# Performance work log

Hardware: AMD Instinct MI355X
Metric: run time of the kernel (lower is better)

Reference implementation:

```python
import jax, jax.numpy as jnp
import numpy as np
import math

B, T, C = 2, 2048, 1024
H = 16
D = C // H


def setup_inputs() -> dict:
    key = jax.random.key(0)
    ks = jax.random.split(key, 5)
    s = 1.0 / math.sqrt(C)
    return {
        "x": jax.random.normal(ks[0], (B, T, C), dtype=jnp.float32),
        "W_qkv": jax.random.normal(ks[1], (C, 3 * C), dtype=jnp.float32) * s,
        "b_qkv": jnp.zeros((3 * C,), dtype=jnp.float32),
        "W_proj": jax.random.normal(ks[2], (C, C), dtype=jnp.float32) * s,
        "b_proj": jnp.zeros((C,), dtype=jnp.float32),
    }


def reference(x, W_qkv, b_qkv, W_proj, b_proj):
    qkv = x @ W_qkv + b_qkv  # [B,T,3C]
    q, k, v = jnp.split(qkv, 3, axis=-1)
    # [B,T,C] -> [B,H,T,D]
    q = q.reshape(B, T, H, D).transpose(0, 2, 1, 3)
    k = k.reshape(B, T, H, D).transpose(0, 2, 1, 3)
    v = v.reshape(B, T, H, D).transpose(0, 2, 1, 3)
    sm_scale = 1.0 / math.sqrt(D)
    att = jnp.einsum("bhqd,bhkd->bhqk", q, k) * sm_scale
    causal = jnp.tril(jnp.ones((T, T), dtype=bool))  # True = keep
    att = jnp.where(causal, att, -jnp.inf)
    att = jax.nn.softmax(att, axis=-1)
    y = jnp.einsum("bhqk,bhkd->bhqd", att, v)  # [B,H,T,D]
    y = y.transpose(0, 2, 1, 3).reshape(B, T, C)
    return y @ W_proj + b_proj
```

## Files before the change

### kernel.cpp

```cpp
#include <hip/hip_runtime.h>
#include <hip/hip_bf16.h>
#include <math.h>

#define BB 2
#define TT 2048
#define CCH 1024
#define HH 16
#define DD 64
#define BT (BB*TT)
#define N3 (3*CCH)

typedef __attribute__((ext_vector_type(8))) short short8;
typedef __attribute__((ext_vector_type(4))) float f32x4;
typedef __attribute__((ext_vector_type(16))) float f32x16;

__device__ __forceinline__ unsigned short f2bf(float f) {
  unsigned int u = __float_as_uint(f);
  unsigned int r = (u + 0x7FFFu + ((u >> 16) & 1u)) >> 16;
  return (unsigned short)r;
}
__device__ __forceinline__ int cvtpk(float lo, float hi) {
  int r;
  asm("v_cvt_pk_bf16_f32 %0, %1, %2" : "=v"(r) : "v"(lo), "v"(hi));
  return r;
}
__device__ __forceinline__ void plswap(int &a, int &b) {
  asm("v_permlane32_swap_b32 %0, %1" : "+v"(a), "+v"(b));
}
__device__ __forceinline__ float fexp2(float x) {
  float r;
  asm("v_exp_f32 %0, %1" : "=v"(r) : "v"(x));
  return r;
}
__device__ __forceinline__ void gload_lds16(const unsigned short* g, unsigned short* l) {
  __builtin_amdgcn_global_load_lds((const __attribute__((address_space(1))) void*)g,
                                   (__attribute__((address_space(3))) void*)l, 16, 0, 0);
}
__device__ __forceinline__ float fmax3(float a, float b, float c) {
  return fmaxf(fmaxf(a, b), c);
}


__global__ __launch_bounds__(256) void k_convert(const float* __restrict__ in,
                                                 unsigned short* __restrict__ out, int n8) {
  int i = blockIdx.x * 256 + threadIdx.x;
  if (i < n8) {
    const float4 a = *(const float4*)(in + (size_t)i * 8);
    const float4 b = *(const float4*)(in + (size_t)i * 8 + 4);
    short8 v;
    v[0] = f2bf(a.x); v[1] = f2bf(a.y); v[2] = f2bf(a.z); v[3] = f2bf(a.w);
    v[4] = f2bf(b.x); v[5] = f2bf(b.y); v[6] = f2bf(b.z); v[7] = f2bf(b.w);
    *(short8*)(out + (size_t)i * 8) = v;
  }
}

__global__ __launch_bounds__(256) void k_transpose_cvt(const float* __restrict__ in,
                                                       unsigned short* __restrict__ out,
                                                       int R, int Cn) {
  __shared__ float tile[32][33];
  int tc = blockIdx.x * 32;
  int tr = blockIdx.y * 32;
  int lx = threadIdx.x & 31;
  int ly = threadIdx.x >> 5;
#pragma unroll
  for (int i = 0; i < 32; i += 8)
    tile[ly + i][lx] = in[(size_t)(tr + ly + i) * Cn + tc + lx];
  __syncthreads();
#pragma unroll
  for (int i = 0; i < 32; i += 8)
    out[(size_t)(tc + ly + i) * R + tr + lx] = f2bf(tile[lx][ly + i]);
}

__global__ __launch_bounds__(256) void k_qkv_gemm(const unsigned short* __restrict__ Xb,
                                                  const unsigned short* __restrict__ Wt,
                                                  const float* __restrict__ bias,
                                                  unsigned short* __restrict__ Qf,
                                                  unsigned short* __restrict__ Kf,
                                                  unsigned short* __restrict__ Vf) {
  __shared__ __align__(16) unsigned short As[128 * 32];
  __shared__ __align__(16) unsigned short Bs[128 * 32];
  int tid = threadIdx.x;
  int mb = blockIdx.x * 128;
  int nb = blockIdx.y * 128;
  int wid = tid >> 6, lane = tid & 63;
  int wr = (wid >> 1) * 64, wc = (wid & 1) * 64;
  int l15 = lane & 15, l4 = lane >> 4;
  int l16 = lane >> 2, lc = (lane & 3) * 8;
  f32x4 acc[4][4];
#pragma unroll
  for (int a = 0; a < 4; ++a)
#pragma unroll
    for (int b = 0; b < 4; ++b)
#pragma unroll
      for (int j = 0; j < 4; ++j) acc[a][b][j] = 0.0f;

  for (int kb = 0; kb < CCH; kb += 32) {
#pragma unroll
    for (int i = 0; i < 2; ++i) {
      int arow = wid * 32 + i * 16;
      gload_lds16(Xb + (size_t)(mb + arow + l16) * CCH + kb + lc, &As[arow * 32]);
      gload_lds16(Wt + (size_t)(nb + arow + l16) * CCH + kb + lc, &Bs[arow * 32]);
    }
    __syncthreads();
    short8 af[4], bfr[4];
#pragma unroll
    for (int mt = 0; mt < 4; ++mt) af[mt] = *(const short8*)(&As[(wr + mt * 16 + l15) * 32 + l4 * 8]);
#pragma unroll
    for (int nt = 0; nt < 4; ++nt) bfr[nt] = *(const short8*)(&Bs[(wc + nt * 16 + l15) * 32 + l4 * 8]);
#pragma unroll
    for (int mt = 0; mt < 4; ++mt)
#pragma unroll
      for (int nt = 0; nt < 4; ++nt)
        acc[mt][nt] = __builtin_amdgcn_mfma_f32_16x16x32_bf16(af[mt], bfr[nt], acc[mt][nt], 0, 0, 0);
    __syncthreads();
  }

#pragma unroll
  for (int mt = 0; mt < 4; ++mt) {
#pragma unroll
    for (int nt = 0; nt < 4; ++nt) {
      int gcol = nb + wc + nt * 16 + l15;
      int which = gcol >> 10;
      int cc = gcol & 1023;
      int hh = cc >> 6, d = cc & 63;
      float bv = bias[gcol];
#pragma unroll
      for (int j = 0; j < 4; ++j) {
        int grow = mb + wr + mt * 16 + l4 * 4 + j;
        int b = grow >> 11, t = grow & 2047;
        float v = acc[mt][nt][j] + bv;
        size_t bh = (size_t)(b * HH + hh) * TT * DD;
        if (which == 2) {
          size_t a = (size_t)((((t >> 6) * 2 + (d >> 5)) * 4 + ((t >> 4) & 3)) * 512
                             + (((t >> 3) & 1) * 32 + (d & 31)) * 8 + (t & 7));
          Vf[bh + a] = f2bf(v);
        } else {
          size_t a = (size_t)(((t >> 5) * 4 + (d >> 4)) * 512
                             + ((d >> 3) & 1) * 256 + (t & 31) * 8 + (d & 7));
          if (which == 0) Qf[bh + a] = f2bf(v * 0.18033688f);
          else            Kf[bh + a] = f2bf(v);
        }
      }
    }
  }
}

__global__ __launch_bounds__(128) void k_attn(const unsigned short* __restrict__ Qf,
                                              const unsigned short* __restrict__ Kf,
                                              const unsigned short* __restrict__ Vf,
                                              unsigned short* __restrict__ Y) {
  __shared__ float ex[64 * 33];
  __shared__ float exml[128];
  int tid = threadIdx.x;
  int jx = blockIdx.x;
  int j = 63 - (jx >> 5);
  int bh = jx & 31;
  int wid = tid >> 6, lane = tid & 63;
  int l31 = lane & 31, h = lane >> 5;
  int q0 = j * 32;
  int qrow = q0 + l31;
  int tmax = j >> 1;

  const unsigned short* Qp = Qf + (size_t)bh * TT * DD;
  const unsigned short* Kp = Kf + (size_t)bh * TT * DD;
  const unsigned short* Vp = Vf + (size_t)bh * TT * DD;

  short8 qf[4];
#pragma unroll
  for (int m = 0; m < 4; ++m)
    qf[m] = *(const short8*)(Qp + (size_t)(j * 4 + m) * 512 + lane * 8);

  f32x16 zv;
#pragma unroll
  for (int r = 0; r < 16; ++r) zv[r] = 0.0f;
  f32x16 po[2];
  po[0] = zv; po[1] = zv;
  float mrun = -1e30f, lrun = 0.0f;

  for (int t = wid; t <= tmax; t += 2) {
    int kvb = t * 64;

    short8 kf[2][4];
#pragma unroll
    for (int t32 = 0; t32 < 2; ++t32)
#pragma unroll
      for (int m = 0; m < 4; ++m)
        kf[t32][m] = *(const short8*)(Kp + (size_t)((t * 2 + t32) * 4 + m) * 512 + lane * 8);

    f32x16 st[2];
    __builtin_amdgcn_s_setprio(1);
#pragma unroll
    for (int t32 = 0; t32 < 2; ++t32) {
      st[t32] = __builtin_amdgcn_mfma_f32_32x32x16_bf16(kf[t32][0], qf[0], zv, 0, 0, 0);
#pragma unroll
      for (int m = 1; m < 4; ++m)
        st[t32] = __builtin_amdgcn_mfma_f32_32x32x16_bf16(kf[t32][m], qf[m], st[t32], 0, 0, 0);
    }
    __builtin_amdgcn_s_setprio(0);

    short8 vf[2][4];
#pragma unroll
    for (int dt = 0; dt < 2; ++dt)
#pragma unroll
      for (int g = 0; g < 4; ++g)
        vf[dt][g] = *(const short8*)(Vp + (size_t)((t * 2 + dt) * 4 + g) * 512 + lane * 8);

    if (kvb + 63 > q0) {
#pragma unroll
      for (int t32 = 0; t32 < 2; ++t32)
#pragma unroll
        for (int r = 0; r < 16; ++r) {
          int kvg = kvb + t32 * 32 + (r & 3) + 8 * (r >> 2) + 4 * h;
          if (kvg > qrow) st[t32][r] = -1e30f;
        }
    }

    float A = st[0][0], B = st[0][1], C = st[0][2], Dv = st[0][3];
#pragma unroll
    for (int r = 4; r < 16; r += 4) {
      A = fmax3(A, st[0][r], st[0][r + 1]);
      B = fmax3(B, st[0][r + 2], st[0][r + 3]);
      C = fmax3(C, st[1][r - 4], st[1][r - 3]);
      Dv = fmax3(Dv, st[1][r - 2], st[1][r - 1]);
    }
    C = fmax3(C, st[1][12], st[1][13]);
    Dv = fmax3(Dv, st[1][14], st[1][15]);
    float mx = fmaxf(fmax3(A, B, C), Dv);
    mx = fmaxf(mx, __shfl_xor(mx, 32));

    if (__any(mx - mrun > 8.0f)) {
      float mnew = fmaxf(mrun, mx);
      float alpha = fexp2(mrun - mnew);
      lrun *= alpha;
#pragma unroll
      for (int dt = 0; dt < 2; ++dt)
#pragma unroll
        for (int r = 0; r < 16; ++r) po[dt][r] *= alpha;
      mrun = mnew;
    }

    float sum = 0.0f;
#pragma unroll
    for (int t32 = 0; t32 < 2; ++t32)
#pragma unroll
      for (int r = 0; r < 16; ++r) {
        float p = fexp2(st[t32][r] - mrun);
        st[t32][r] = p;
        sum += p;
      }
    sum += __shfl_xor(sum, 32);
    lrun += sum;

    short8 pf[4];
#pragma unroll
    for (int g = 0; g < 4; ++g) {
      int t32 = g >> 1, r0 = (g & 1) * 8;
      int a = cvtpk(st[t32][r0 + 0], st[t32][r0 + 1]);
      int b = cvtpk(st[t32][r0 + 4], st[t32][r0 + 5]);
      plswap(a, b);
      int c = cvtpk(st[t32][r0 + 2], st[t32][r0 + 3]);
      int d = cvtpk(st[t32][r0 + 6], st[t32][r0 + 7]);
      plswap(c, d);
      union { int w[4]; short8 s; } un;
      un.w[0] = a; un.w[1] = c; un.w[2] = b; un.w[3] = d;
      pf[g] = un.s;
    }

    __builtin_amdgcn_s_setprio(1);
#pragma unroll
    for (int dt = 0; dt < 2; ++dt)
#pragma unroll
      for (int g = 0; g < 4; ++g)
        po[dt] = __builtin_amdgcn_mfma_f32_32x32x16_bf16(vf[dt][g], pf[g], po[dt], 0, 0, 0);
    __builtin_amdgcn_s_setprio(0);
  }

  __syncthreads();
  if (wid == 1) {
#pragma unroll
    for (int dt = 0; dt < 2; ++dt)
#pragma unroll
      for (int r = 0; r < 16; ++r) ex[lane * 33 + dt * 16 + r] = po[dt][r];
    exml[lane] = mrun;
    exml[64 + lane] = lrun;
  }
  __syncthreads();
  if (wid == 0) {
    float m1 = exml[lane], l1 = exml[64 + lane];
    float M = fmaxf(mrun, m1);
    float a0 = fexp2(mrun - M), a1 = fexp2(m1 - M);
    float inv = 1.0f / (lrun * a0 + l1 * a1);
    a0 *= inv; a1 *= inv;
    int b = bh >> 4, hh = bh & 15;
    unsigned short* yp = Y + ((size_t)(b * TT + qrow)) * CCH + hh * DD;
#pragma unroll
    for (int dt = 0; dt < 2; ++dt)
#pragma unroll
      for (int r = 0; r < 16; r += 2) {
        int d = dt * 32 + (r & 3) + 8 * (r >> 2) + 4 * h;
        float v0 = po[dt][r]     * a0 + ex[lane * 33 + dt * 16 + r]     * a1;
        float v1 = po[dt][r + 1] * a0 + ex[lane * 33 + dt * 16 + r + 1] * a1;
        *(int*)(yp + d) = cvtpk(v0, v1);
      }
  }
}

__global__ __launch_bounds__(256) void k_proj_gemm(const unsigned short* __restrict__ Yb,
                                                   const unsigned short* __restrict__ Wt,
                                                   const float* __restrict__ bias,
                                                   float* __restrict__ Out) {
  __shared__ __align__(16) unsigned short As[128 * 32];
  __shared__ __align__(16) unsigned short Bs[128 * 32];
  int tid = threadIdx.x;
  int mb = blockIdx.x * 128;
  int nb = blockIdx.y * 128;
  int wid = tid >> 6, lane = tid & 63;
  int wr = (wid >> 1) * 64, wc = (wid & 1) * 64;
  int l15 = lane & 15, l4 = lane >> 4;
  int l16 = lane >> 2, lc = (lane & 3) * 8;
  f32x4 acc[4][4];
#pragma unroll
  for (int a = 0; a < 4; ++a)
#pragma unroll
    for (int b = 0; b < 4; ++b)
#pragma unroll
      for (int j = 0; j < 4; ++j) acc[a][b][j] = 0.0f;

  for (int kb = 0; kb < CCH; kb += 32) {
#pragma unroll
    for (int i = 0; i < 2; ++i) {
      int arow = wid * 32 + i * 16;
      gload_lds16(Yb + (size_t)(mb + arow + l16) * CCH + kb + lc, &As[arow * 32]);
      gload_lds16(Wt + (size_t)(nb + arow + l16) * CCH + kb + lc, &Bs[arow * 32]);
    }
    __syncthreads();
    short8 af[4], bfr[4];
#pragma unroll
    for (int mt = 0; mt < 4; ++mt) af[mt] = *(const short8*)(&As[(wr + mt * 16 + l15) * 32 + l4 * 8]);
#pragma unroll
    for (int nt = 0; nt < 4; ++nt) bfr[nt] = *(const short8*)(&Bs[(wc + nt * 16 + l15) * 32 + l4 * 8]);
#pragma unroll
    for (int mt = 0; mt < 4; ++mt)
#pragma unroll
      for (int nt = 0; nt < 4; ++nt)
        acc[mt][nt] = __builtin_amdgcn_mfma_f32_16x16x32_bf16(af[mt], bfr[nt], acc[mt][nt], 0, 0, 0);
    __syncthreads();
  }

#pragma unroll
  for (int mt = 0; mt < 4; ++mt) {
#pragma unroll
    for (int nt = 0; nt < 4; ++nt) {
      int gcol = nb + wc + nt * 16 + l15;
      float bv = bias[gcol];
#pragma unroll
      for (int j = 0; j < 4; ++j) {
        int grow = mb + wr + mt * 16 + l4 * 4 + j;
        Out[(size_t)grow * CCH + gcol] = acc[mt][nt][j] + bv;
      }
    }
  }
}

extern "C" void kernel_launch(void* const* d_in, const int* in_sizes, int n_in,
                              void* d_out, int out_size, void* d_ws, size_t ws_size,
                              hipStream_t stream) {
  const float* x      = (const float*)d_in[0];
  const float* W_qkv  = (const float*)d_in[1];
  const float* b_qkv  = (const float*)d_in[2];
  const float* W_proj = (const float*)d_in[3];
  const float* b_proj = (const float*)d_in[4];
  float* out = (float*)d_out;

  char* ws = (char*)d_ws;
  size_t off = 0;
  unsigned short* Wt_qkv  = (unsigned short*)(ws + off); off += (size_t)N3 * CCH * 2;
  unsigned short* Wt_proj = (unsigned short*)(ws + off); off += (size_t)CCH * CCH * 2;
  unsigned short* Xb      = (unsigned short*)(ws + off); off += (size_t)BT * CCH * 2;
  unsigned short* Qfb     = (unsigned short*)(ws + off); off += (size_t)BT * CCH * 2;
  unsigned short* Kfb     = (unsigned short*)(ws + off); off += (size_t)BT * CCH * 2;
  unsigned short* Vfb     = (unsigned short*)(ws + off); off += (size_t)BT * CCH * 2;
  unsigned short* Yb      = (unsigned short*)(ws + off); off += (size_t)BT * CCH * 2;

  k_convert<<<dim3(BT * CCH / 8 / 256), 256, 0, stream>>>(x, Xb, BT * CCH / 8);
  k_transpose_cvt<<<dim3(N3 / 32, CCH / 32), 256, 0, stream>>>(W_qkv, Wt_qkv, CCH, N3);
  k_transpose_cvt<<<dim3(CCH / 32, CCH / 32), 256, 0, stream>>>(W_proj, Wt_proj, CCH, CCH);
  k_qkv_gemm<<<dim3(BT / 128, N3 / 128), 256, 0, stream>>>(Xb, Wt_qkv, b_qkv, Qfb, Kfb, Vfb);
  k_attn<<<dim3(2048), 128, 0, stream>>>(Qfb, Kfb, Vfb, Yb);
  k_proj_gemm<<<dim3(BT / 128, CCH / 128), 256, 0, stream>>>(Yb, Wt_proj, b_proj, out);
}
```

Measured before the change: 109.4 us.

## Deepen GEMM K-tile to 64 with XOR-swizzled LDS and block swizzle

Both the QKV and projection GEMMs now stage 64-wide K slices instead of 32, which halves the number of barrier-separated iterations. The LDS layout is XOR-swizzled on both the global-to-LDS load and the fragment reads to avoid bank conflicts. Block indices are remapped in groups of 8 to improve L2 reuse of the operand tiles. Costs are double the shared memory per block and more fragment registers, which may lower occupancy.

```diff
diff --git a/kernel.cpp b/kernel.cpp
--- a/kernel.cpp
+++ b/kernel.cpp
@@ -77,15 +77,18 @@
                                                   unsigned short* __restrict__ Qf,
                                                   unsigned short* __restrict__ Kf,
                                                   unsigned short* __restrict__ Vf) {
-  __shared__ __align__(16) unsigned short As[128 * 32];
-  __shared__ __align__(16) unsigned short Bs[128 * 32];
+  __shared__ __align__(16) unsigned short As[128 * 64];
+  __shared__ __align__(16) unsigned short Bs[128 * 64];
   int tid = threadIdx.x;
-  int mb = blockIdx.x * 128;
-  int nb = blockIdx.y * 128;
+  int id = blockIdx.y * gridDim.x + blockIdx.x;
+  int swz = (id & 7) * 96 + (id >> 3);
+  int mb = (swz & 31) * 128;
+  int nb = (swz >> 5) * 128;
   int wid = tid >> 6, lane = tid & 63;
   int wr = (wid >> 1) * 64, wc = (wid & 1) * 64;
   int l15 = lane & 15, l4 = lane >> 4;
-  int l16 = lane >> 2, lc = (lane & 3) * 8;
+  int r8 = lane >> 3, c8 = lane & 7;
+  int csw = ((c8 ^ r8) * 8);
   f32x4 acc[4][4];
 #pragma unroll
   for (int a = 0; a < 4; ++a)
@@ -94,24 +97,36 @@
 #pragma unroll
       for (int j = 0; j < 4; ++j) acc[a][b][j] = 0.0f;
 
-  for (int kb = 0; kb < CCH; kb += 32) {
-#pragma unroll
-    for (int i = 0; i < 2; ++i) {
-      int arow = wid * 32 + i * 16;
-      gload_lds16(Xb + (size_t)(mb + arow + l16) * CCH + kb + lc, &As[arow * 32]);
-      gload_lds16(Wt + (size_t)(nb + arow + l16) * CCH + kb + lc, &Bs[arow * 32]);
+  for (int kb = 0; kb < CCH; kb += 64) {
+#pragma unroll
+    for (int i = 0; i < 4; ++i) {
+      int brow = wid * 32 + i * 8;
+      gload_lds16(Xb + (size_t)(mb + brow + r8) * CCH + kb + csw, &As[brow * 64]);
+      gload_lds16(Wt + (size_t)(nb + brow + r8) * CCH + kb + csw, &Bs[brow * 64]);
     }
     __syncthreads();
-    short8 af[4], bfr[4];
-#pragma unroll
-    for (int mt = 0; mt < 4; ++mt) af[mt] = *(const short8*)(&As[(wr + mt * 16 + l15) * 32 + l4 * 8]);
-#pragma unroll
-    for (int nt = 0; nt < 4; ++nt) bfr[nt] = *(const short8*)(&Bs[(wc + nt * 16 + l15) * 32 + l4 * 8]);
-#pragma unroll
-    for (int mt = 0; mt < 4; ++mt)
-#pragma unroll
-      for (int nt = 0; nt < 4; ++nt)
-        acc[mt][nt] = __builtin_amdgcn_mfma_f32_16x16x32_bf16(af[mt], bfr[nt], acc[mt][nt], 0, 0, 0);
+    short8 af[2][4], bfr[2][4];
+#pragma unroll
+    for (int ks = 0; ks < 2; ++ks) {
+#pragma unroll
+      for (int mt = 0; mt < 4; ++mt) {
+        int row = wr + mt * 16 + l15;
+        af[ks][mt] = *(const short8*)(&As[row * 64 + (((ks * 4 + l4) ^ (row & 7)) * 8)]);
+      }
+#pragma unroll
+      for (int nt = 0; nt < 4; ++nt) {
+        int row = wc + nt * 16 + l15;
+        bfr[ks][nt] = *(const short8*)(&Bs[row * 64 + (((ks * 4 + l4) ^ (row & 7)) * 8)]);
+      }
+    }
+#pragma unroll
+    for (int ks = 0; ks < 2; ++ks)
+#pragma unroll
+      for (int mt = 0; mt < 4; ++mt)
+#pragma unroll
+        for (int nt = 0; nt < 4; ++nt)
+          acc[mt][nt] = __builtin_amdgcn_mfma_f32_16x16x32_bf16(af[ks][mt], bfr[ks][nt],
+                                                                acc[mt][nt], 0, 0, 0);
     __syncthreads();
   }
 
@@ -309,15 +324,18 @@
                                                    const unsigned short* __restrict__ Wt,
                                                    const float* __restrict__ bias,
                                                    float* __restrict__ Out) {
-  __shared__ __align__(16) unsigned short As[128 * 32];
-  __shared__ __align__(16) unsigned short Bs[128 * 32];
+  __shared__ __align__(16) unsigned short As[128 * 64];
+  __shared__ __align__(16) unsigned short Bs[128 * 64];
   int tid = threadIdx.x;
-  int mb = blockIdx.x * 128;
-  int nb = blockIdx.y * 128;
+  int id = blockIdx.y * gridDim.x + blockIdx.x;
+  int swz = (id & 7) * 32 + (id >> 3);
+  int mb = (swz & 31) * 128;
+  int nb = (swz >> 5) * 128;
   int wid = tid >> 6, lane = tid & 63;
   int wr = (wid >> 1) * 64, wc = (wid & 1) * 64;
   int l15 = lane & 15, l4 = lane >> 4;
-  int l16 = lane >> 2, lc = (lane & 3) * 8;
+  int r8 = lane >> 3, c8 = lane & 7;
+  int csw = ((c8 ^ r8) * 8);
   f32x4 acc[4][4];
 #pragma unroll
   for (int a = 0; a < 4; ++a)
@@ -326,24 +344,36 @@
 #pragma unroll
       for (int j = 0; j < 4; ++j) acc[a][b][j] = 0.0f;
 
-  for (int kb = 0; kb < CCH; kb += 32) {
-#pragma unroll
-    for (int i = 0; i < 2; ++i) {
-      int arow = wid * 32 + i * 16;
-      gload_lds16(Yb + (size_t)(mb + arow + l16) * CCH + kb + lc, &As[arow * 32]);
-      gload_lds16(Wt + (size_t)(nb + arow + l16) * CCH + kb + lc, &Bs[arow * 32]);
+  for (int kb = 0; kb < CCH; kb += 64) {
+#pragma unroll
+    for (int i = 0; i < 4; ++i) {
+      int brow = wid * 32 + i * 8;
+      gload_lds16(Yb + (size_t)(mb + brow + r8) * CCH + kb + csw, &As[brow * 64]);
+      gload_lds16(Wt + (size_t)(nb + brow + r8) * CCH + kb + csw, &Bs[brow * 64]);
     }
     __syncthreads();
-    short8 af[4], bfr[4];
-#pragma unroll
-    for (int mt = 0; mt < 4; ++mt) af[mt] = *(const short8*)(&As[(wr + mt * 16 + l15) * 32 + l4 * 8]);
-#pragma unroll
-    for (int nt = 0; nt < 4; ++nt) bfr[nt] = *(const short8*)(&Bs[(wc + nt * 16 + l15) * 32 + l4 * 8]);
-#pragma unroll
-    for (int mt = 0; mt < 4; ++mt)
-#pragma unroll
-      for (int nt = 0; nt < 4; ++nt)
-        acc[mt][nt] = __builtin_amdgcn_mfma_f32_16x16x32_bf16(af[mt], bfr[nt], acc[mt][nt], 0, 0, 0);
+    short8 af[2][4], bfr[2][4];
+#pragma unroll
+    for (int ks = 0; ks < 2; ++ks) {
+#pragma unroll
+      for (int mt = 0; mt < 4; ++mt) {
+        int row = wr + mt * 16 + l15;
+        af[ks][mt] = *(const short8*)(&As[row * 64 + (((ks * 4 + l4) ^ (row & 7)) * 8)]);
+      }
+#pragma unroll
+      for (int nt = 0; nt < 4; ++nt) {
+        int row = wc + nt * 16 + l15;
+        bfr[ks][nt] = *(const short8*)(&Bs[row * 64 + (((ks * 4 + l4) ^ (row & 7)) * 8)]);
+      }
+    }
+#pragma unroll
+    for (int ks = 0; ks < 2; ++ks)
+#pragma unroll
+      for (int mt = 0; mt < 4; ++mt)
+#pragma unroll
+        for (int nt = 0; nt < 4; ++nt)
+          acc[mt][nt] = __builtin_amdgcn_mfma_f32_16x16x32_bf16(af[ks][mt], bfr[ks][nt],
+                                                                acc[mt][nt], 0, 0, 0);
     __syncthreads();
   }
 
```

Result: slower. 126.4 us (+15.5%).

## Triple-buffer LDS tiles in QKV and projection GEMMs with async prefetch

Applied to the files above, without the earlier changes.

The QKV and output-projection GEMM main loops now use a three-stage LDS ring buffer. The next K-tile is issued via direct global-to-LDS loads before computing on the current one, with a partial vmcnt wait and one barrier per iteration instead of two __syncthreads. This is meant to hide global load latency behind MFMA work and cut synchronisation per K step. The cost is triple the LDS footprint (48KB per block), which may lower occupancy. Correctness depends on the three-deep ring keeping a write from landing on a buffer other waves are still reading.

```diff
diff --git a/kernel.cpp b/kernel.cpp
--- a/kernel.cpp
+++ b/kernel.cpp
@@ -77,8 +77,8 @@
                                                   unsigned short* __restrict__ Qf,
                                                   unsigned short* __restrict__ Kf,
                                                   unsigned short* __restrict__ Vf) {
-  __shared__ __align__(16) unsigned short As[128 * 32];
-  __shared__ __align__(16) unsigned short Bs[128 * 32];
+  __shared__ __align__(16) unsigned short As[3][128 * 32];
+  __shared__ __align__(16) unsigned short Bs[3][128 * 32];
   int tid = threadIdx.x;
   int mb = blockIdx.x * 128;
   int nb = blockIdx.y * 128;
@@ -94,25 +94,41 @@
 #pragma unroll
       for (int j = 0; j < 4; ++j) acc[a][b][j] = 0.0f;
 
+#pragma unroll
+  for (int i = 0; i < 2; ++i) {
+    int arow = wid * 32 + i * 16;
+    gload_lds16(Xb + (size_t)(mb + arow + l16) * CCH + lc, &As[0][arow * 32]);
+    gload_lds16(Wt + (size_t)(nb + arow + l16) * CCH + lc, &Bs[0][arow * 32]);
+  }
+
+  int buf = 0;
   for (int kb = 0; kb < CCH; kb += 32) {
-#pragma unroll
-    for (int i = 0; i < 2; ++i) {
-      int arow = wid * 32 + i * 16;
-      gload_lds16(Xb + (size_t)(mb + arow + l16) * CCH + kb + lc, &As[arow * 32]);
-      gload_lds16(Wt + (size_t)(nb + arow + l16) * CCH + kb + lc, &Bs[arow * 32]);
-    }
-    __syncthreads();
+    int nxt = buf + 1; if (nxt == 3) nxt = 0;
+    if (kb + 32 < CCH) {
+#pragma unroll
+      for (int i = 0; i < 2; ++i) {
+        int arow = wid * 32 + i * 16;
+        gload_lds16(Xb + (size_t)(mb + arow + l16) * CCH + kb + 32 + lc, &As[nxt][arow * 32]);
+        gload_lds16(Wt + (size_t)(nb + arow + l16) * CCH + kb + 32 + lc, &Bs[nxt][arow * 32]);
+      }
+      asm volatile("s_waitcnt vmcnt(4)" ::: "memory");
+    } else {
+      asm volatile("s_waitcnt vmcnt(0)" ::: "memory");
+    }
+    __builtin_amdgcn_s_barrier();
+    __builtin_amdgcn_sched_barrier(0);
+
     short8 af[4], bfr[4];
 #pragma unroll
-    for (int mt = 0; mt < 4; ++mt) af[mt] = *(const short8*)(&As[(wr + mt * 16 + l15) * 32 + l4 * 8]);
-#pragma unroll
-    for (int nt = 0; nt < 4; ++nt) bfr[nt] = *(const short8*)(&Bs[(wc + nt * 16 + l15) * 32 + l4 * 8]);
+    for (int mt = 0; mt < 4; ++mt) af[mt] = *(const short8*)(&As[buf][(wr + mt * 16 + l15) * 32 + l4 * 8]);
+#pragma unroll
+    for (int nt = 0; nt < 4; ++nt) bfr[nt] = *(const short8*)(&Bs[buf][(wc + nt * 16 + l15) * 32 + l4 * 8]);
 #pragma unroll
     for (int mt = 0; mt < 4; ++mt)
 #pragma unroll
       for (int nt = 0; nt < 4; ++nt)
         acc[mt][nt] = __builtin_amdgcn_mfma_f32_16x16x32_bf16(af[mt], bfr[nt], acc[mt][nt], 0, 0, 0);
-    __syncthreads();
+    buf = nxt;
   }
 
 #pragma unroll
@@ -309,8 +325,8 @@
                                                    const unsigned short* __restrict__ Wt,
                                                    const float* __restrict__ bias,
                                                    float* __restrict__ Out) {
-  __shared__ __align__(16) unsigned short As[128 * 32];
-  __shared__ __align__(16) unsigned short Bs[128 * 32];
+  __shared__ __align__(16) unsigned short As[3][128 * 32];
+  __shared__ __align__(16) unsigned short Bs[3][128 * 32];
   int tid = threadIdx.x;
   int mb = blockIdx.x * 128;
   int nb = blockIdx.y * 128;
@@ -326,25 +342,41 @@
 #pragma unroll
       for (int j = 0; j < 4; ++j) acc[a][b][j] = 0.0f;
 
+#pragma unroll
+  for (int i = 0; i < 2; ++i) {
+    int arow = wid * 32 + i * 16;
+    gload_lds16(Yb + (size_t)(mb + arow + l16) * CCH + lc, &As[0][arow * 32]);
+    gload_lds16(Wt + (size_t)(nb + arow + l16) * CCH + lc, &Bs[0][arow * 32]);
+  }
+
+  int buf = 0;
   for (int kb = 0; kb < CCH; kb += 32) {
-#pragma unroll
-    for (int i = 0; i < 2; ++i) {
-      int arow = wid * 32 + i * 16;
-      gload_lds16(Yb + (size_t)(mb + arow + l16) * CCH + kb + lc, &As[arow * 32]);
-      gload_lds16(Wt + (size_t)(nb + arow + l16) * CCH + kb + lc, &Bs[arow * 32]);
-    }
-    __syncthreads();
+    int nxt = buf + 1; if (nxt == 3) nxt = 0;
+    if (kb + 32 < CCH) {
+#pragma unroll
+      for (int i = 0; i < 2; ++i) {
+        int arow = wid * 32 + i * 16;
+        gload_lds16(Yb + (size_t)(mb + arow + l16) * CCH + kb + 32 + lc, &As[nxt][arow * 32]);
+        gload_lds16(Wt + (size_t)(nb + arow + l16) * CCH + kb + 32 + lc, &Bs[nxt][arow * 32]);
+      }
+      asm volatile("s_waitcnt vmcnt(4)" ::: "memory");
+    } else {
+      asm volatile("s_waitcnt vmcnt(0)" ::: "memory");
+    }
+    __builtin_amdgcn_s_barrier();
+    __builtin_amdgcn_sched_barrier(0);
+
     short8 af[4], bfr[4];
 #pragma unroll
-    for (int mt = 0; mt < 4; ++mt) af[mt] = *(const short8*)(&As[(wr + mt * 16 + l15) * 32 + l4 * 8]);
-#pragma unroll
-    for (int nt = 0; nt < 4; ++nt) bfr[nt] = *(const short8*)(&Bs[(wc + nt * 16 + l15) * 32 + l4 * 8]);
+    for (int mt = 0; mt < 4; ++mt) af[mt] = *(const short8*)(&As[buf][(wr + mt * 16 + l15) * 32 + l4 * 8]);
+#pragma unroll
+    for (int nt = 0; nt < 4; ++nt) bfr[nt] = *(const short8*)(&Bs[buf][(wc + nt * 16 + l15) * 32 + l4 * 8]);
 #pragma unroll
     for (int mt = 0; mt < 4; ++mt)
 #pragma unroll
       for (int nt = 0; nt < 4; ++nt)
         acc[mt][nt] = __builtin_amdgcn_mfma_f32_16x16x32_bf16(af[mt], bfr[nt], acc[mt][nt], 0, 0, 0);
-    __syncthreads();
+    buf = nxt;
   }
 
 #pragma unroll
```

Result: no change. 111.0 us (+1.4%).
